# Performance work log

Hardware: AMD Instinct MI355X
Metric: run time of the kernel (lower is better)

Reference implementation:

```python
import jax, jax.numpy as jnp
import numpy as np


def setup_inputs() -> dict:
    key = jax.random.key(0)
    ks = jax.random.split(key, 5)
    B, C, H, W = 4, 512, 64, 64
    A = 64  # attention_features
    s = lambda fan_in: 1.0 / np.sqrt(fan_in)
    return {
        "x": jax.random.normal(ks[0], (B, C, H, W), dtype=jnp.float32),
        "Wf": jax.random.normal(ks[1], (C, A), dtype=jnp.float32) * s(C),
        "bf": jnp.zeros((A,), dtype=jnp.float32),
        "Wg": jax.random.normal(ks[2], (C, A), dtype=jnp.float32) * s(C),
        "bg": jnp.zeros((A,), dtype=jnp.float32),
        "Wh": jax.random.normal(ks[3], (C, C), dtype=jnp.float32) * s(C),
        "bh": jnp.zeros((C,), dtype=jnp.float32),
        "scale": jax.random.uniform(ks[4], (), dtype=jnp.float32),
    }


def reference(x, Wf, bf, Wg, bg, Wh, bh, scale):
    B, C, H, W = x.shape
    N = H * W

    def conv1x1(w, b):  # 1x1 conv == per-pixel matmul over channels
        return jnp.einsum('bchw,cf->bfhw', x, w) + b[None, :, None, None]

    f = conv1x1(Wf, bf)  # [B, A, H, W]
    g = conv1x1(Wg, bg)  # [B, A, H, W]
    h = conv1x1(Wh, bh)  # [B, C, H, W]

    # flatten_hw (channels_first): [B, C', H, W] -> [B, N, C']
    flat = lambda t: t.reshape(B, t.shape[1], N).transpose(0, 2, 1)
    gf = flat(g)  # [B, N, A]
    ff = flat(f)  # [B, N, A]
    hf = flat(h)  # [B, N, C]

    s = jnp.einsum('bnd,bmd->bnm', gf, ff)       # [B, N, N]
    attn = jax.nn.softmax(s, axis=-1)
    o = jnp.einsum('bnm,bmc->bnc', attn, hf)     # [B, N, C]
    # Original does a raw reshape back to x's shape (no transpose) — keep it.
    y = scale * o.reshape(x.shape) + x
    return y
```

## Files before the change

### kernel.cpp

```cpp
#include <hip/hip_runtime.h>
#include <hip/hip_bf16.h>

constexpr int BB = 4;
constexpr int C  = 512;
constexpr int A  = 64;
constexpr int N  = 4096;

typedef __attribute__((ext_vector_type(8))) short s16x8;
typedef __attribute__((ext_vector_type(4))) float f32x4;

#define MFMA_16x16x32_BF16(a, b, c) __builtin_amdgcn_mfma_f32_16x16x32_bf16((a), (b), (c), 0, 0, 0)

typedef __attribute__((address_space(3))) unsigned int lds_u32_t;
typedef const __attribute__((address_space(1))) unsigned int glb_u32_t;

__device__ __forceinline__ void gl2lds16(const void* g, void* l) {
    __builtin_amdgcn_global_load_lds((glb_u32_t*)g, (lds_u32_t*)l, 16, 0, 0);
}

__global__ __launch_bounds__(256) void k_trans(const float* __restrict__ src,
                                               __hip_bfloat16* __restrict__ dst,
                                               int K, int M) {
    __shared__ __hip_bfloat16 Ls[64][66];
    int m0 = blockIdx.x << 6, k0 = blockIdx.y << 6;
    size_t bo = (size_t)blockIdx.z * K * M;
    int t = threadIdx.x;
    int lm = t & 63, g = t >> 6;
    #pragma unroll
    for (int j = 0; j < 16; ++j) {
        int kk = j * 4 + g;
        Ls[kk][lm] = __float2bfloat16(src[bo + (size_t)(k0 + kk) * M + m0 + lm]);
    }
    __syncthreads();
    #pragma unroll
    for (int j = 0; j < 16; ++j) {
        int mm = j * 4 + g;
        dst[bo + (size_t)(m0 + mm) * K + k0 + lm] = Ls[lm][mm];
    }
}

__global__ __launch_bounds__(256) void k_trans2(const float* __restrict__ src,
                                                __hip_bfloat16* __restrict__ dhi,
                                                __hip_bfloat16* __restrict__ dlo,
                                                int K, int M) {
    __shared__ float Ls[64][65];
    int m0 = blockIdx.x << 6, k0 = blockIdx.y << 6;
    size_t bo = (size_t)blockIdx.z * K * M;
    int t = threadIdx.x;
    int lm = t & 63, g = t >> 6;
    #pragma unroll
    for (int j = 0; j < 16; ++j) {
        int kk = j * 4 + g;
        Ls[kk][lm] = src[bo + (size_t)(k0 + kk) * M + m0 + lm];
    }
    __syncthreads();
    #pragma unroll
    for (int j = 0; j < 16; ++j) {
        int mm = j * 4 + g;
        float v = Ls[lm][mm];
        __hip_bfloat16 h = __float2bfloat16(v);
        size_t idx = bo + (size_t)(m0 + mm) * K + k0 + lm;
        dhi[idx] = h;
        dlo[idx] = __float2bfloat16(v - __bfloat162float(h));
    }
}

__global__ __launch_bounds__(256) void k_fgm(const __hip_bfloat16* __restrict__ XThi, const __hip_bfloat16* __restrict__ XTlo,
                                             const __hip_bfloat16* __restrict__ WfThi, const __hip_bfloat16* __restrict__ WfTlo,
                                             const __hip_bfloat16* __restrict__ WgThi, const __hip_bfloat16* __restrict__ WgTlo,
                                             const float* __restrict__ bfv, const float* __restrict__ bgv,
                                             __hip_bfloat16* __restrict__ FFhi, __hip_bfloat16* __restrict__ FFlo,
                                             __hip_bfloat16* __restrict__ GFhi, __hip_bfloat16* __restrict__ GFlo) {
    __shared__ __align__(16) __hip_bfloat16 Ah[64 * 32], Al[64 * 32];
    __shared__ __align__(16) __hip_bfloat16 Bh[128 * 32], Bl[128 * 32];
    int r0 = blockIdx.x << 6;
    int t = threadIdx.x;
    int w = t >> 6, l = t & 63;
    int ln15 = l & 15, quad = l >> 4;
    int mh = w & 1, nh = w >> 1;

    f32x4 acc[2][4];
    #pragma unroll
    for (int mi = 0; mi < 2; ++mi)
        #pragma unroll
        for (int ni = 0; ni < 4; ++ni) acc[mi][ni] = (f32x4){0.f, 0.f, 0.f, 0.f};

    for (int kt = 0; kt < C; kt += 32) {
        {
            int row = t >> 2, seg = t & 3;
            int gseg = (seg - (row >> 1)) & 3;
            size_t go = (size_t)(r0 + row) * C + kt + gseg * 8;
            gl2lds16(XThi + go, &Ah[t * 8]);
            gl2lds16(XTlo + go, &Al[t * 8]);
        }
        #pragma unroll
        for (int j = 0; j < 2; ++j) {
            int i = j * 256 + t;
            int row = i >> 2, seg = i & 3;
            int gseg = (seg - (row >> 1)) & 3;
            size_t go = (size_t)(row & 63) * C + kt + gseg * 8;
            const __hip_bfloat16* bh = j ? WgThi : WfThi;
            const __hip_bfloat16* bl = j ? WgTlo : WfTlo;
            gl2lds16(bh + go, &Bh[i * 8]);
            gl2lds16(bl + go, &Bl[i * 8]);
        }
        __syncthreads();
        s16x8 afh[2], afl[2], bfh[4], bfl[4];
        #pragma unroll
        for (int mi = 0; mi < 2; ++mi) {
            int row = mh * 32 + mi * 16 + ln15;
            int sw = ((quad + (row >> 1)) & 3) << 3;
            afh[mi] = *(const s16x8*)&Ah[row * 32 + sw];
            afl[mi] = *(const s16x8*)&Al[row * 32 + sw];
        }
        #pragma unroll
        for (int ni = 0; ni < 4; ++ni) {
            int row = nh * 64 + ni * 16 + ln15;
            int sw = ((quad + (row >> 1)) & 3) << 3;
            bfh[ni] = *(const s16x8*)&Bh[row * 32 + sw];
            bfl[ni] = *(const s16x8*)&Bl[row * 32 + sw];
        }
        #pragma unroll
        for (int mi = 0; mi < 2; ++mi)
            #pragma unroll
            for (int ni = 0; ni < 4; ++ni) {
                acc[mi][ni] = MFMA_16x16x32_BF16(afh[mi], bfh[ni], acc[mi][ni]);
                acc[mi][ni] = MFMA_16x16x32_BF16(afl[mi], bfh[ni], acc[mi][ni]);
                acc[mi][ni] = MFMA_16x16x32_BF16(afh[mi], bfl[ni], acc[mi][ni]);
            }
        __syncthreads();
    }

    #pragma unroll
    for (int mi = 0; mi < 2; ++mi) {
        #pragma unroll
        for (int r = 0; r < 4; ++r) {
            size_t grow = (size_t)(r0 + mh * 32 + mi * 16 + quad * 4 + r) * A;
            #pragma unroll
            for (int ni = 0; ni < 4; ++ni) {
                int col = nh * 64 + ni * 16 + ln15;
                if (col < A) {
                    float v = acc[mi][ni][r] + bfv[col];
                    __hip_bfloat16 h = __float2bfloat16(v);
                    FFhi[grow + col] = h;
                    FFlo[grow + col] = __float2bfloat16(v - __bfloat162float(h));
                } else {
                    int a = col - A;
                    float v = acc[mi][ni][r] + bgv[a];
                    __hip_bfloat16 h = __float2bfloat16(v);
                    GFhi[grow + a] = h;
                    GFlo[grow + a] = __float2bfloat16(v - __bfloat162float(h));
                }
            }
        }
    }
}

__global__ __launch_bounds__(256) void k_hm(const __hip_bfloat16* __restrict__ WhT,
                                            const __hip_bfloat16* __restrict__ XT,
                                            const float* __restrict__ bhv,
                                            __hip_bfloat16* __restrict__ HFT) {
    __shared__ __align__(16) __hip_bfloat16 As[128 * 32];
    __shared__ __align__(16) __hip_bfloat16 Bs[128 * 32];
    int b  = blockIdx.z;
    int c0 = blockIdx.x << 7;
    int n0 = blockIdx.y << 7;
    int t = threadIdx.x;
    int w = t >> 6, l = t & 63;
    int ln15 = l & 15, quad = l >> 4;
    int mc = (w >> 1) << 6, nn = (w & 1) << 6;

    const __hip_bfloat16* Bb = XT + (size_t)b * N * C;

    f32x4 acc[4][4];
    #pragma unroll
    for (int mi = 0; mi < 4; ++mi)
        #pragma unroll
        for (int ni = 0; ni < 4; ++ni) acc[mi][ni] = (f32x4){0.f, 0.f, 0.f, 0.f};

    for (int kt = 0; kt < C; kt += 32) {
        #pragma unroll
        for (int j = 0; j < 2; ++j) {
            int i = j * 256 + t;
            int row = i >> 2, seg = i & 3;
            int gseg = (seg - (row >> 1)) & 3;
            gl2lds16(WhT + ((size_t)(c0 + row) * C + kt + gseg * 8), &As[i * 8]);
        }
        #pragma unroll
        for (int j = 0; j < 2; ++j) {
            int i = j * 256 + t;
            int row = i >> 2, seg = i & 3;
            int gseg = (seg - (row >> 1)) & 3;
            gl2lds16(Bb + ((size_t)(n0 + row) * C + kt + gseg * 8), &Bs[i * 8]);
        }
        __syncthreads();
        s16x8 af[4], bf2[4];
        #pragma unroll
        for (int mi = 0; mi < 4; ++mi) {
            int row = mc + mi * 16 + ln15;
            int sw = ((quad + (row >> 1)) & 3) << 3;
            af[mi] = *(const s16x8*)&As[row * 32 + sw];
        }
        #pragma unroll
        for (int ni = 0; ni < 4; ++ni) {
            int row = nn + ni * 16 + ln15;
            int sw = ((quad + (row >> 1)) & 3) << 3;
            bf2[ni] = *(const s16x8*)&Bs[row * 32 + sw];
        }
        #pragma unroll
        for (int mi = 0; mi < 4; ++mi)
            #pragma unroll
            for (int ni = 0; ni < 4; ++ni)
                acc[mi][ni] = MFMA_16x16x32_BF16(af[mi], bf2[ni], acc[mi][ni]);
        __syncthreads();
    }

    #pragma unroll
    for (int mi = 0; mi < 4; ++mi) {
        #pragma unroll
        for (int r = 0; r < 4; ++r) {
            int c = c0 + mc + mi * 16 + quad * 4 + r;
            float bias = bhv[c];
            size_t rowbase = ((size_t)b * C + c) * N;
            #pragma unroll
            for (int ni = 0; ni < 4; ++ni) {
                int n = n0 + nn + ni * 16 + ln15;
                HFT[rowbase + n] = __float2bfloat16(acc[mi][ni][r] + bias);
            }
        }
    }
}

__global__ __launch_bounds__(512) void k_s(const __hip_bfloat16* __restrict__ GFhi, const __hip_bfloat16* __restrict__ GFlo,
                                           const __hip_bfloat16* __restrict__ FFhi, const __hip_bfloat16* __restrict__ FFlo,
                                           __hip_bfloat16* __restrict__ P, float* __restrict__ rowsum) {
    __shared__ __align__(16) __hip_bfloat16 Fsh[2][128 * 32];
    __shared__ __align__(16) __hip_bfloat16 Fsl[2][128 * 32];
    __shared__ float sred[8][32];
    int b = blockIdx.y;
    int q0 = blockIdx.x << 6;
    int t = threadIdx.x;
    int w = t >> 6, l = t & 63;
    int ln15 = l & 15, quad = l >> 4, q8 = quad << 3;
    int qh = w & 1, kq = w >> 1;
    int qbase = q0 + qh * 32;

    const __hip_bfloat16* Fh = FFhi + (size_t)b * N * A;
    const __hip_bfloat16* Fl = FFlo + (size_t)b * N * A;
    __hip_bfloat16* Pb = P + (size_t)b * N * N;

    s16x8 ah[2][2], al[2][2];
    #pragma unroll
    for (int m = 0; m < 2; ++m) {
        const __hip_bfloat16* gp = GFhi + ((size_t)(b * N + qbase + m * 16 + ln15)) * A + q8;
        const __hip_bfloat16* lp = GFlo + ((size_t)(b * N + qbase + m * 16 + ln15)) * A + q8;
        ah[m][0] = *(const s16x8*)gp; ah[m][1] = *(const s16x8*)(gp + 32);
        al[m][0] = *(const s16x8*)lp; al[m][1] = *(const s16x8*)(lp + 32);
    }

    int srow = t >> 2;
    int sseg = ((t & 3) - (srow >> 1)) & 3;
    size_t sgoff0 = (size_t)srow * A + sseg * 8;

    float sm[2][4] = {{0.f,0.f,0.f,0.f},{0.f,0.f,0.f,0.f}};
    for (int kt = 0; kt < N; kt += 128) {
        gl2lds16(Fh + (size_t)kt * A + sgoff0,      &Fsh[0][t * 8]);
        gl2lds16(Fh + (size_t)kt * A + 32 + sgoff0, &Fsh[1][t * 8]);
        gl2lds16(Fl + (size_t)kt * A + sgoff0,      &Fsl[0][t * 8]);
        gl2lds16(Fl + (size_t)kt * A + 32 + sgoff0, &Fsl[1][t * 8]);
        __syncthreads();
        #pragma unroll
        for (int s = 0; s < 2; ++s) {
            int sub = kq * 2 + s;
            int ro = sub * 16 + ln15;
            int sw = ((quad + (ro >> 1)) & 3) << 3;
            s16x8 kh0 = *(const s16x8*)&Fsh[0][ro * 32 + sw];
            s16x8 kh1 = *(const s16x8*)&Fsh[1][ro * 32 + sw];
            s16x8 kl0 = *(const s16x8*)&Fsl[0][ro * 32 + sw];
            s16x8 kl1 = *(const s16x8*)&Fsl[1][ro * 32 + sw];
            int key = kt + sub * 16 + ln15;
            #pragma unroll
            for (int m = 0; m < 2; ++m) {
                f32x4 acc = {0.f, 0.f, 0.f, 0.f};
                acc = MFMA_16x16x32_BF16(ah[m][0], kh0, acc);
                acc = MFMA_16x16x32_BF16(ah[m][1], kh1, acc);
                acc = MFMA_16x16x32_BF16(al[m][0], kh0, acc);
                acc = MFMA_16x16x32_BF16(al[m][1], kh1, acc);
                acc = MFMA_16x16x32_BF16(ah[m][0], kl0, acc);
                acc = MFMA_16x16x32_BF16(ah[m][1], kl1, acc);
                size_t prow = (size_t)(qbase + m * 16 + quad * 4) * N + key;
                #pragma unroll
                for (int r = 0; r < 4; ++r) {
                    float p = __expf(acc[r]);
                    __hip_bfloat16 pb = __float2bfloat16(p);
                    sm[m][r] += __bfloat162float(pb);
                    Pb[prow + (size_t)r * N] = pb;
                }
            }
        }
        __syncthreads();
    }
    #pragma unroll
    for (int d = 1; d < 16; d <<= 1)
        #pragma unroll
        for (int m = 0; m < 2; ++m)
            #pragma unroll
            for (int r = 0; r < 4; ++r) sm[m][r] += __shfl_xor(sm[m][r], d, 64);
    if (ln15 == 0) {
        #pragma unroll
        for (int m = 0; m < 2; ++m)
            #pragma unroll
            for (int r = 0; r < 4; ++r) sred[w][m * 16 + quad * 4 + r] = sm[m][r];
    }
    __syncthreads();
    if (t < 64) {
        int hq = t >> 5, row = t & 31;
        rowsum[b * N + q0 + t] = sred[hq][row] + sred[hq + 2][row] +
                                 sred[hq + 4][row] + sred[hq + 6][row];
    }
}

__global__ __launch_bounds__(256) void k_o(const __hip_bfloat16* __restrict__ P,
                                           const __hip_bfloat16* __restrict__ HFT,
                                           const float* __restrict__ rowsum,
                                           const float* __restrict__ x,
                                           const float* __restrict__ scalep,
                                           float* __restrict__ out) {
    __shared__ __align__(16) __hip_bfloat16 As[128 * 32];
    __shared__ __align__(16) __hip_bfloat16 Bs[128 * 32];
    int id = blockIdx.x;
    int cb   = (id >> 3) & 3;
    int rest = (id & 7) | ((id >> 5) << 3);
    int qs = rest & 31, b = rest >> 5;
    int q0 = qs << 7, c0 = cb << 7;
    int t = threadIdx.x;
    int w = t >> 6, l = t & 63;
    int ln15 = l & 15, quad = l >> 4;
    int mq = (w >> 1) << 6, nc = (w & 1) << 6;

    const __hip_bfloat16* Ab = P   + (size_t)b * N * N;
    const __hip_bfloat16* Bb = HFT + (size_t)b * C * N;

    f32x4 acc[4][4];
    #pragma unroll
    for (int mi = 0; mi < 4; ++mi)
        #pragma unroll
        for (int ni = 0; ni < 4; ++ni) acc[mi][ni] = (f32x4){0.f, 0.f, 0.f, 0.f};

    for (int kt = 0; kt < N; kt += 32) {
        #pragma unroll
        for (int j = 0; j < 2; ++j) {
            int i = j * 256 + t;
            int row = i >> 2, seg = i & 3;
            int gseg = (seg - (row >> 1)) & 3;
            gl2lds16(Ab + ((size_t)(q0 + row) * N + kt + gseg * 8), &As[i * 8]);
        }
        #pragma unroll
        for (int j = 0; j < 2; ++j) {
            int i = j * 256 + t;
            int row = i >> 2, seg = i & 3;
            int gseg = (seg - (row >> 1)) & 3;
            gl2lds16(Bb + ((size_t)(c0 + row) * N + kt + gseg * 8), &Bs[i * 8]);
        }
        __syncthreads();
        s16x8 af[4], bf2[4];
        #pragma unroll
        for (int mi = 0; mi < 4; ++mi) {
            int row = mq + mi * 16 + ln15;
            int sw = ((quad + (row >> 1)) & 3) << 3;
            af[mi] = *(const s16x8*)&As[row * 32 + sw];
        }
        #pragma unroll
        for (int ni = 0; ni < 4; ++ni) {
            int row = nc + ni * 16 + ln15;
            int sw = ((quad + (row >> 1)) & 3) << 3;
            bf2[ni] = *(const s16x8*)&Bs[row * 32 + sw];
        }
        #pragma unroll
        for (int mi = 0; mi < 4; ++mi)
            #pragma unroll
            for (int ni = 0; ni < 4; ++ni)
                acc[mi][ni] = MFMA_16x16x32_BF16(af[mi], bf2[ni], acc[mi][ni]);
        __syncthreads();
    }

    float scv = *scalep;
    #pragma unroll
    for (int mi = 0; mi < 4; ++mi) {
        #pragma unroll
        for (int r = 0; r < 4; ++r) {
            int q = q0 + mq + mi * 16 + quad * 4 + r;
            float srs = scv / rowsum[b * N + q];
            size_t rowbase = (size_t)b * N * C + (size_t)q * C;
            #pragma unroll
            for (int ni = 0; ni < 4; ++ni) {
                size_t idx = rowbase + (size_t)(c0 + nc + ni * 16 + ln15);
                out[idx] = acc[mi][ni][r] * srs + x[idx];
            }
        }
    }
}

extern "C" void kernel_launch(void* const* d_in, const int* in_sizes, int n_in,
                              void* d_out, int out_size, void* d_ws, size_t ws_size,
                              hipStream_t stream) {
    const float* x   = (const float*)d_in[0];
    const float* Wf  = (const float*)d_in[1];
    const float* bfv = (const float*)d_in[2];
    const float* Wg  = (const float*)d_in[3];
    const float* bgv = (const float*)d_in[4];
    const float* Wh  = (const float*)d_in[5];
    const float* bhv = (const float*)d_in[6];
    const float* sc  = (const float*)d_in[7];
    float* out = (float*)d_out;

    char* ws = (char*)d_ws;
    size_t off = 0;
    __hip_bfloat16* FFhi = (__hip_bfloat16*)(ws + off); off += (size_t)BB * N * A * 2;
    __hip_bfloat16* FFlo = (__hip_bfloat16*)(ws + off); off += (size_t)BB * N * A * 2;
    __hip_bfloat16* GFhi = (__hip_bfloat16*)(ws + off); off += (size_t)BB * N * A * 2;
    __hip_bfloat16* GFlo = (__hip_bfloat16*)(ws + off); off += (size_t)BB * N * A * 2;
    __hip_bfloat16* HFT  = (__hip_bfloat16*)(ws + off); off += (size_t)BB * C * N * 2;
    char* Pbase          = (ws + off);                  off += (size_t)BB * N * N * 2;
    __hip_bfloat16* P    = (__hip_bfloat16*)Pbase;
    float* rowsum        = (float*)(ws + off);          off += (size_t)BB * N * 4;
    __hip_bfloat16* WhT  = (__hip_bfloat16*)(ws + off); off += (size_t)C * C * 2;
    __hip_bfloat16* WfThi = (__hip_bfloat16*)(ws + off); off += (size_t)A * C * 2;
    __hip_bfloat16* WfTlo = (__hip_bfloat16*)(ws + off); off += (size_t)A * C * 2;
    __hip_bfloat16* WgThi = (__hip_bfloat16*)(ws + off); off += (size_t)A * C * 2;
    __hip_bfloat16* WgTlo = (__hip_bfloat16*)(ws + off); off += (size_t)A * C * 2;
    __hip_bfloat16* XThi = (__hip_bfloat16*)(Pbase + (size_t)BB * N * N * 2 - (size_t)BB * N * C * 2);
    __hip_bfloat16* XTlo = (__hip_bfloat16*)(Pbase + (size_t)BB * N * N * 2 - 2 * (size_t)BB * N * C * 2);

    k_trans<<<dim3(C / 64, C / 64, 1), dim3(256), 0, stream>>>(Wh, WhT, C, C);
    k_trans2<<<dim3(N / 64, C / 64, BB), dim3(256), 0, stream>>>(x, XThi, XTlo, C, N);
    k_trans2<<<dim3(A / 64, C / 64, 1), dim3(256), 0, stream>>>(Wf, WfThi, WfTlo, C, A);
    k_trans2<<<dim3(A / 64, C / 64, 1), dim3(256), 0, stream>>>(Wg, WgThi, WgTlo, C, A);
    k_hm<<<dim3(C / 128, N / 128, BB), dim3(256), 0, stream>>>(WhT, XThi, bhv, HFT);
    k_fgm<<<dim3((BB * N) / 64), dim3(256), 0, stream>>>(XThi, XTlo, WfThi, WfTlo, WgThi, WgTlo,
                                                         bfv, bgv, FFhi, FFlo, GFhi, GFlo);
    k_s<<<dim3(N / 64, BB), dim3(512), 0, stream>>>(GFhi, GFlo, FFhi, FFlo, P, rowsum);
    k_o<<<dim3(512), dim3(256), 0, stream>>>(P, HFT, rowsum, x, sc, out);
}
```

Before: 295.8 us.

## Transpose S-tile MFMA for packed P stores and shrink k_o query tile

In k_s, the MFMA operands are swapped so each lane holds four consecutive keys of one query row. That lets it pack four bf16 probabilities into a single 8-byte store instead of four strided 2-byte stores, and the row-sum reduction shrinks to two shuffles. In k_o, the query tile drops from 128 to 64 rows, doubling the grid to 1024 blocks and adding a launch-bounds occupancy hint of 4, to improve occupancy and CU balance. The cost is less reuse of the HFT tile per block, so more global/L2 traffic for the B operand.

```diff
diff --git a/kernel.cpp b/kernel.cpp
--- a/kernel.cpp
+++ b/kernel.cpp
@@ -262,7 +262,7 @@
     int sseg = ((t & 3) - (srow >> 1)) & 3;
     size_t sgoff0 = (size_t)srow * A + sseg * 8;
 
-    float sm[2][4] = {{0.f,0.f,0.f,0.f},{0.f,0.f,0.f,0.f}};
+    float sm[2] = {0.f, 0.f};
     for (int kt = 0; kt < N; kt += 128) {
         gl2lds16(Fh + (size_t)kt * A + sgoff0,      &Fsh[0][t * 8]);
         gl2lds16(Fh + (size_t)kt * A + 32 + sgoff0, &Fsh[1][t * 8]);
@@ -278,39 +278,40 @@
             s16x8 kh1 = *(const s16x8*)&Fsh[1][ro * 32 + sw];
             s16x8 kl0 = *(const s16x8*)&Fsl[0][ro * 32 + sw];
             s16x8 kl1 = *(const s16x8*)&Fsl[1][ro * 32 + sw];
-            int key = kt + sub * 16 + ln15;
+            int key0 = kt + sub * 16 + quad * 4;
             #pragma unroll
             for (int m = 0; m < 2; ++m) {
                 f32x4 acc = {0.f, 0.f, 0.f, 0.f};
-                acc = MFMA_16x16x32_BF16(ah[m][0], kh0, acc);
-                acc = MFMA_16x16x32_BF16(ah[m][1], kh1, acc);
-                acc = MFMA_16x16x32_BF16(al[m][0], kh0, acc);
-                acc = MFMA_16x16x32_BF16(al[m][1], kh1, acc);
-                acc = MFMA_16x16x32_BF16(ah[m][0], kl0, acc);
-                acc = MFMA_16x16x32_BF16(ah[m][1], kl1, acc);
-                size_t prow = (size_t)(qbase + m * 16 + quad * 4) * N + key;
-                #pragma unroll
-                for (int r = 0; r < 4; ++r) {
-                    float p = __expf(acc[r]);
-                    __hip_bfloat16 pb = __float2bfloat16(p);
-                    sm[m][r] += __bfloat162float(pb);
-                    Pb[prow + (size_t)r * N] = pb;
+                acc = MFMA_16x16x32_BF16(kh0, ah[m][0], acc);
+                acc = MFMA_16x16x32_BF16(kh1, ah[m][1], acc);
+                acc = MFMA_16x16x32_BF16(kh0, al[m][0], acc);
+                acc = MFMA_16x16x32_BF16(kh1, al[m][1], acc);
+                acc = MFMA_16x16x32_BF16(kl0, ah[m][0], acc);
+                acc = MFMA_16x16x32_BF16(kl1, ah[m][1], acc);
+                ushort4 pk;
+                {
+                    float p0 = __expf(acc[0]); __hip_bfloat16 b0 = __float2bfloat16(p0);
+                    float p1 = __expf(acc[1]); __hip_bfloat16 b1 = __float2bfloat16(p1);
+                    float p2 = __expf(acc[2]); __hip_bfloat16 b2 = __float2bfloat16(p2);
+                    float p3 = __expf(acc[3]); __hip_bfloat16 b3 = __float2bfloat16(p3);
+                    sm[m] += __bfloat162float(b0) + __bfloat162float(b1)
+                           + __bfloat162float(b2) + __bfloat162float(b3);
+                    pk.x = *(unsigned short*)&b0; pk.y = *(unsigned short*)&b1;
+                    pk.z = *(unsigned short*)&b2; pk.w = *(unsigned short*)&b3;
                 }
+                *(ushort4*)&Pb[(size_t)(qbase + m * 16 + ln15) * N + key0] = pk;
             }
         }
         __syncthreads();
     }
     #pragma unroll
-    for (int d = 1; d < 16; d <<= 1)
-        #pragma unroll
-        for (int m = 0; m < 2; ++m)
-            #pragma unroll
-            for (int r = 0; r < 4; ++r) sm[m][r] += __shfl_xor(sm[m][r], d, 64);
-    if (ln15 == 0) {
-        #pragma unroll
-        for (int m = 0; m < 2; ++m)
-            #pragma unroll
-            for (int r = 0; r < 4; ++r) sred[w][m * 16 + quad * 4 + r] = sm[m][r];
+    for (int m = 0; m < 2; ++m) {
+        sm[m] += __shfl_xor(sm[m], 16, 64);
+        sm[m] += __shfl_xor(sm[m], 32, 64);
+    }
+    if (quad == 0) {
+        sred[w][ln15]      = sm[0];
+        sred[w][16 + ln15] = sm[1];
     }
     __syncthreads();
     if (t < 64) {
@@ -320,64 +321,62 @@
     }
 }
 
-__global__ __launch_bounds__(256) void k_o(const __hip_bfloat16* __restrict__ P,
-                                           const __hip_bfloat16* __restrict__ HFT,
-                                           const float* __restrict__ rowsum,
-                                           const float* __restrict__ x,
-                                           const float* __restrict__ scalep,
-                                           float* __restrict__ out) {
-    __shared__ __align__(16) __hip_bfloat16 As[128 * 32];
+__global__ __launch_bounds__(256, 4) void k_o(const __hip_bfloat16* __restrict__ P,
+                                              const __hip_bfloat16* __restrict__ HFT,
+                                              const float* __restrict__ rowsum,
+                                              const float* __restrict__ x,
+                                              const float* __restrict__ scalep,
+                                              float* __restrict__ out) {
+    __shared__ __align__(16) __hip_bfloat16 As[64 * 32];
     __shared__ __align__(16) __hip_bfloat16 Bs[128 * 32];
     int id = blockIdx.x;
     int cb   = (id >> 3) & 3;
     int rest = (id & 7) | ((id >> 5) << 3);
-    int qs = rest & 31, b = rest >> 5;
-    int q0 = qs << 7, c0 = cb << 7;
+    int qs = rest & 63, b = rest >> 6;
+    int q0 = qs << 6, c0 = cb << 7;
     int t = threadIdx.x;
     int w = t >> 6, l = t & 63;
     int ln15 = l & 15, quad = l >> 4;
-    int mq = (w >> 1) << 6, nc = (w & 1) << 6;
+    int wq = w & 1, wc = w >> 1;
 
     const __hip_bfloat16* Ab = P   + (size_t)b * N * N;
     const __hip_bfloat16* Bb = HFT + (size_t)b * C * N;
 
-    f32x4 acc[4][4];
-    #pragma unroll
-    for (int mi = 0; mi < 4; ++mi)
+    f32x4 acc[2][4];
+    #pragma unroll
+    for (int mi = 0; mi < 2; ++mi)
         #pragma unroll
         for (int ni = 0; ni < 4; ++ni) acc[mi][ni] = (f32x4){0.f, 0.f, 0.f, 0.f};
 
     for (int kt = 0; kt < N; kt += 32) {
+        {
+            int row = t >> 2, seg = t & 3;
+            int gseg = (seg - (row >> 1)) & 3;
+            gl2lds16(Ab + ((size_t)(q0 + row) * N + kt + gseg * 8), &As[t * 8]);
+        }
         #pragma unroll
         for (int j = 0; j < 2; ++j) {
             int i = j * 256 + t;
             int row = i >> 2, seg = i & 3;
             int gseg = (seg - (row >> 1)) & 3;
-            gl2lds16(Ab + ((size_t)(q0 + row) * N + kt + gseg * 8), &As[i * 8]);
-        }
-        #pragma unroll
-        for (int j = 0; j < 2; ++j) {
-            int i = j * 256 + t;
-            int row = i >> 2, seg = i & 3;
-            int gseg = (seg - (row >> 1)) & 3;
             gl2lds16(Bb + ((size_t)(c0 + row) * N + kt + gseg * 8), &Bs[i * 8]);
         }
         __syncthreads();
-        s16x8 af[4], bf2[4];
-        #pragma unroll
-        for (int mi = 0; mi < 4; ++mi) {
-            int row = mq + mi * 16 + ln15;
+        s16x8 af[2], bf2[4];
+        #pragma unroll
+        for (int mi = 0; mi < 2; ++mi) {
+            int row = wq * 32 + mi * 16 + ln15;
             int sw = ((quad + (row >> 1)) & 3) << 3;
             af[mi] = *(const s16x8*)&As[row * 32 + sw];
         }
         #pragma unroll
         for (int ni = 0; ni < 4; ++ni) {
-            int row = nc + ni * 16 + ln15;
+            int row = wc * 64 + ni * 16 + ln15;
             int sw = ((quad + (row >> 1)) & 3) << 3;
             bf2[ni] = *(const s16x8*)&Bs[row * 32 + sw];
         }
         #pragma unroll
-        for (int mi = 0; mi < 4; ++mi)
+        for (int mi = 0; mi < 2; ++mi)
             #pragma unroll
             for (int ni = 0; ni < 4; ++ni)
                 acc[mi][ni] = MFMA_16x16x32_BF16(af[mi], bf2[ni], acc[mi][ni]);
@@ -386,15 +385,15 @@
 
     float scv = *scalep;
     #pragma unroll
-    for (int mi = 0; mi < 4; ++mi) {
+    for (int mi = 0; mi < 2; ++mi) {
         #pragma unroll
         for (int r = 0; r < 4; ++r) {
-            int q = q0 + mq + mi * 16 + quad * 4 + r;
+            int q = q0 + wq * 32 + mi * 16 + quad * 4 + r;
             float srs = scv / rowsum[b * N + q];
             size_t rowbase = (size_t)b * N * C + (size_t)q * C;
             #pragma unroll
             for (int ni = 0; ni < 4; ++ni) {
-                size_t idx = rowbase + (size_t)(c0 + nc + ni * 16 + ln15);
+                size_t idx = rowbase + (size_t)(c0 + wc * 64 + ni * 16 + ln15);
                 out[idx] = acc[mi][ni][r] * srs + x[idx];
             }
         }
@@ -440,5 +439,5 @@
     k_fgm<<<dim3((BB * N) / 64), dim3(256), 0, stream>>>(XThi, XTlo, WfThi, WfTlo, WgThi, WgTlo,
                                                          bfv, bgv, FFhi, FFlo, GFhi, GFlo);
     k_s<<<dim3(N / 64, BB), dim3(512), 0, stream>>>(GFhi, GFlo, FFhi, FFlo, P, rowsum);
-    k_o<<<dim3(512), dim3(256), 0, stream>>>(P, HFT, rowsum, x, sc, out);
-}
+    k_o<<<dim3(1024), dim3(256), 0, stream>>>(P, HFT, rowsum, x, sc, out);
+}
```

New measurement: 321.1 us. +8.6%, slower.
